# Kernel tuning notes

Hardware: AMD Instinct MI355X
Metric: run time of the kernel (lower is better)

## Reference

```python
import jax, jax.numpy as jnp
import numpy as np

N_NODES = 50000
N_EDGES = 800000
EMBED_ROWS = 100000
NUM_RELS = 16
NUM_BASES = 4
FEAT_DIM = 32
OUT_DIM = 32
ATTN_DIM = 32


def setup_inputs() -> dict:
    key = jax.random.key(0)
    ks = jax.random.split(key, 16)
    inp = {
        'feat': jax.random.normal(ks[0], (N_NODES, FEAT_DIM), jnp.float32),
        'embed_table': jax.random.normal(ks[1], (EMBED_ROWS, FEAT_DIM), jnp.float32),
        'transform': jax.random.normal(ks[2], (FEAT_DIM * 2, OUT_DIM), jnp.float32) * 0.1,
        'weight': jax.random.normal(ks[3], (NUM_BASES, OUT_DIM, OUT_DIM), jnp.float32) * 0.1,
        'w_comp': jax.random.normal(ks[4], (NUM_RELS, NUM_BASES), jnp.float32) * 0.5,
        'self_loop_weight': jax.random.normal(ks[5], (OUT_DIM, OUT_DIM), jnp.float32) * 0.1,
        'A_w': jax.random.normal(ks[6], (2 * OUT_DIM + ATTN_DIM, OUT_DIM), jnp.float32) * 0.1,
        'A_b': jax.random.normal(ks[7], (OUT_DIM,), jnp.float32) * 0.1,
        'B_w': jax.random.normal(ks[8], (OUT_DIM, 1), jnp.float32) * 0.1,
        'B_b': jax.random.normal(ks[9], (1,), jnp.float32) * 0.1,
        'attn_emb': jax.random.normal(ks[10], (NUM_RELS, ATTN_DIM), jnp.float32),
        'idx': jax.random.randint(ks[11], (N_NODES,), 0, EMBED_ROWS, jnp.int32),
        'edge_src': jax.random.randint(ks[12], (N_EDGES,), 0, N_NODES, jnp.int32),
        'edge_dst': jax.random.randint(ks[13], (N_EDGES,), 0, N_NODES, jnp.int32),
        'edge_type': jax.random.randint(ks[14], (N_EDGES,), 0, NUM_RELS, jnp.int32),
    }
    return inp


def reference(feat, embed_table, transform, weight, w_comp, self_loop_weight,
              A_w, A_b, B_w, B_b, attn_emb, idx, edge_src, edge_dst, edge_type):
    n = feat.shape[0]
    # input-layer features: concat(feat, embed[idx]) @ transform -> init_fea [N, D]
    init_fea = jnp.concatenate([feat, embed_table[idx]], axis=1) @ transform
    # basis decomposition: rel_w [R, D, D]
    rel_w = jnp.einsum('rb,bio->rio', w_comp, weight)
    # per-edge gather (is_input_layer & add_transe_emb -> x=src init_fea, y=dst init_fea)
    x = init_fea[edge_src]                      # [E, D]
    y = init_fea[edge_dst]                      # [E, D]
    w_e = rel_w[edge_type]                      # [E, D, D]
    msg = jnp.einsum('ed,edo->eo', x, w_e)      # per-edge bmm (edge weight w = 1)
    # attention MLP: a = sigmoid(B(relu(A([x, y, rel_emb]))))
    e = jnp.concatenate([x, y, attn_emb[edge_type]], axis=1)  # [E, 2D+A]
    a = jax.nn.sigmoid(jax.nn.relu(e @ A_w + A_b) @ B_w + B_b)  # [E, 1]
    # scatter-reduce: h_v = curr_emb_v + sum_{e: dst=v} a_e * msg_e
    agg = jax.ops.segment_sum(a * msg, edge_dst, num_segments=n)
    curr = init_fea @ self_loop_weight
    h = jax.nn.relu(curr + agg)  # activation=relu, bias=None, dropout=0
    # is_input_layer & add_transe_emb: repr = concat(init_fea, h) -> [N, 2, D]
    return jnp.stack([init_fea, h], axis=1)
```

## Files before the change

kernel.cpp:

```cpp
#include <hip/hip_runtime.h>
#include <math.h>

#define NN 50000
#define NE 800000
#define NR 16
#define BNODE 64
#define NBC 782
#define ABLK 256
#define CHUNK ((NE + ABLK - 1) / ABLK)
#define NTILE (NE / 16)

typedef __attribute__((ext_vector_type(8))) short short8;
typedef __attribute__((ext_vector_type(4))) float floatx4;

__device__ __forceinline__ unsigned short f2bf(float x) {
    unsigned int u = __float_as_uint(x);
    u += 0x7fffu + ((u >> 16) & 1u);
    return (unsigned short)(u >> 16);
}
__device__ __forceinline__ float bf2f(unsigned short s) {
    return __uint_as_float(((unsigned int)s) << 16);
}

__global__ void __launch_bounds__(256) k_pre(
    const float* __restrict__ feat, const float* __restrict__ emb,
    const float* __restrict__ T, const int* __restrict__ idx,
    const float* __restrict__ weight, const float* __restrict__ A_w,
    const float* __restrict__ A_b, const float* __restrict__ attn_emb,
    const int* __restrict__ ed,
    float* __restrict__ out, unsigned short* __restrict__ init_bf,
    unsigned short* __restrict__ bfrag, unsigned short* __restrict__ afrag,
    float* __restrict__ aproj, int* __restrict__ cpb) {
    if (blockIdx.x >= 260) {
        __shared__ int lc[NBC];
        const int cb = blockIdx.x - 260;
        for (int i = threadIdx.x; i < NBC; i += 256) lc[i] = 0;
        __syncthreads();
        const int start = cb * CHUNK, end = min(start + CHUNK, NE);
        for (int e = start + threadIdx.x; e < end; e += 256)
            atomicAdd(&lc[ed[e] >> 6], 1);
        __syncthreads();
        for (int i = threadIdx.x; i < NBC; i += 256) cpb[cb * NBC + i] = lc[i];
        return;
    }
    if (blockIdx.x < 64) {
        int g = blockIdx.x * 256 + threadIdx.x;
        if (g < 4 * 2 * 64 * 8) {
            int b2 = g >> 10, rest = g & 1023;
            int h = rest >> 9, l = (rest >> 3) & 63, j = rest & 7;
            int k = (l >> 4) * 8 + j, n = (l & 15) + 16 * h;
            bfrag[g] = f2bf(weight[b2 * 1024 + k * 32 + n]);
        }
        if (g < 2 * 2 * 64 * 8) {
            int ks = g >> 10, rest = g & 1023;
            int nt = rest >> 9, l = (rest >> 3) & 63, j = rest & 7;
            int k = ks * 32 + (l >> 4) * 8 + j, n = (l & 15) + 16 * nt;
            afrag[g] = f2bf(A_w[k * 32 + n]);
        }
        if (g < 16 * 32) {
            int t = g >> 5, j = g & 31;
            float acc = A_b[j];
#pragma unroll
            for (int k = 0; k < 32; k++) acc += attn_emb[t * 32 + k] * A_w[(64 + k) * 32 + j];
            aproj[g] = acc;
        }
        return;
    }
    int i = (blockIdx.x - 64) * 256 + threadIdx.x;
    if (i >= NN) return;
    float v[32], acc[32];
#pragma unroll
    for (int o = 0; o < 32; o++) acc[o] = 0.f;
    const float4* fp = (const float4*)(feat + (size_t)i * 32);
#pragma unroll
    for (int q = 0; q < 8; q++) {
        float4 f = fp[q];
        v[4 * q] = f.x; v[4 * q + 1] = f.y; v[4 * q + 2] = f.z; v[4 * q + 3] = f.w;
    }
#pragma unroll
    for (int d = 0; d < 32; d++) {
        float xd = v[d];
#pragma unroll
        for (int o = 0; o < 32; o++) acc[o] += xd * T[d * 32 + o];
    }
    int row = idx[i];
    const float4* ep = (const float4*)(emb + (size_t)row * 32);
#pragma unroll
    for (int q = 0; q < 8; q++) {
        float4 f = ep[q];
        v[4 * q] = f.x; v[4 * q + 1] = f.y; v[4 * q + 2] = f.z; v[4 * q + 3] = f.w;
    }
#pragma unroll
    for (int d = 0; d < 32; d++) {
        float xd = v[d];
#pragma unroll
        for (int o = 0; o < 32; o++) acc[o] += xd * T[(32 + d) * 32 + o];
    }
    float4* op = (float4*)(out + (size_t)i * 64);
#pragma unroll
    for (int q = 0; q < 8; q++) {
        float4 f;
        f.x = acc[4 * q]; f.y = acc[4 * q + 1]; f.z = acc[4 * q + 2]; f.w = acc[4 * q + 3];
        op[q] = f;
    }
    unsigned int w[16];
#pragma unroll
    for (int q = 0; q < 16; q++)
        w[q] = (unsigned int)f2bf(acc[2 * q]) | ((unsigned int)f2bf(acc[2 * q + 1]) << 16);
    uint4* bp = (uint4*)(init_bf + (size_t)i * 32);
#pragma unroll
    for (int q = 0; q < 4; q++) {
        uint4 u; u.x = w[4 * q]; u.y = w[4 * q + 1]; u.z = w[4 * q + 2]; u.w = w[4 * q + 3];
        bp[q] = u;
    }
}

__global__ void __launch_bounds__(256) k_scan1(const int* __restrict__ cpb,
                                               int* __restrict__ cpbx,
                                               int* __restrict__ tot) {
    int bin = blockIdx.x * 256 + threadIdx.x;
    if (bin >= NBC) return;
    int run = 0;
#pragma unroll 8
    for (int c = 0; c < ABLK; c++) {
        int v = cpb[c * NBC + bin];
        cpbx[c * NBC + bin] = run;
        run += v;
    }
    tot[bin] = run;
}

__global__ void __launch_bounds__(1024) k_scan2(const int* __restrict__ tot,
                                                int* __restrict__ boff) {
    __shared__ int ls[1024];
    int t = threadIdx.x;
    int v = (t < NBC) ? tot[t] : 0;
    ls[t] = v;
    __syncthreads();
    for (int off = 1; off < 1024; off <<= 1) {
        int u = (t >= off) ? ls[t - off] : 0;
        __syncthreads();
        ls[t] += u;
        __syncthreads();
    }
    if (t < NBC) boff[t] = ls[t] - v;
    if (t == NBC - 1) boff[NBC] = ls[t];
}

__global__ void __launch_bounds__(1024) k_scatA(const int* __restrict__ es,
                                                const int* __restrict__ ed,
                                                const int* __restrict__ et,
                                                const int* __restrict__ cpbx,
                                                const int* __restrict__ boff,
                                                int* __restrict__ bpack) {
    __shared__ int cur[NBC];
    const int start = blockIdx.x * CHUNK, end = min(start + CHUNK, NE);
    for (int i = threadIdx.x; i < NBC; i += 1024)
        cur[i] = boff[i] + cpbx[blockIdx.x * NBC + i];
    __syncthreads();
    for (int e = start + threadIdx.x; e < end; e += 1024) {
        int s = es[e], d = ed[e], t = et[e];
        int slot = atomicAdd(&cur[d >> 6], 1);
        bpack[slot] = s | ((d & 63) << 16) | (t << 22);
    }
}

__global__ void __launch_bounds__(256) k_fine(const int* __restrict__ boff,
                                              const int* __restrict__ bpack,
                                              int* __restrict__ row_off,
                                              int* __restrict__ e1,
                                              unsigned short* __restrict__ e2) {
    __shared__ int h[BNODE], ls[BNODE], cur[BNODE];
    const int b = blockIdx.x, tid = threadIdx.x;
    const int s0 = boff[b], s1 = boff[b + 1];
    if (tid < BNODE) h[tid] = 0;
    __syncthreads();
    for (int s = s0 + tid; s < s1; s += 256)
        atomicAdd(&h[(bpack[s] >> 16) & 63], 1);
    __syncthreads();
    if (tid < BNODE) ls[tid] = h[tid];
    __syncthreads();
    for (int off = 1; off < BNODE; off <<= 1) {
        int u = (tid < BNODE && tid >= off) ? ls[tid - off] : 0;
        __syncthreads();
        if (tid < BNODE) ls[tid] += u;
        __syncthreads();
    }
    if (tid < BNODE) {
        int excl = ls[tid] - h[tid];
        int node = b * BNODE + tid;
        if (node <= NN) row_off[node] = s0 + excl;
        cur[tid] = s0 + excl;
    }
    __syncthreads();
    for (int s = s0 + tid; s < s1; s += 256) {
        int pk = bpack[s];
        int f = (pk >> 16) & 63;
        int p = atomicAdd(&cur[f], 1);
        e1[p] = (pk & 0xffff) | (((pk >> 22) & 15) << 16);
        e2[p] = (unsigned short)(b * BNODE + f);
    }
}

__global__ void __launch_bounds__(256) k_msg(
    const unsigned short* __restrict__ bfrag, const unsigned short* __restrict__ afrag,
    const float* __restrict__ aproj, const float* __restrict__ w_comp,
    const float* __restrict__ B_w, const float* __restrict__ B_b,
    const int* __restrict__ e1, const unsigned short* __restrict__ e2,
    const unsigned short* __restrict__ init_bf, unsigned short* __restrict__ amsg) {
    const int wave = threadIdx.x >> 6;
    const int lane = threadIdx.x & 63;
    const int ti = blockIdx.x * 4 + wave;
    const int m = lane & 15, quad = lane >> 4;
    const int e = ti * 16 + m;
    const int ev = e1[e];
    const int src = ev & 0xffff;
    const int dst = e2[e];
    short8 xa = *(const short8*)(init_bf + (size_t)src * 32 + quad * 8);
    short8 ya = *(const short8*)(init_bf + (size_t)dst * 32 + quad * 8);
    const short8* bfp = (const short8*)bfrag;
    const short8* afp = (const short8*)afrag;
    floatx4 z4 = {0.f, 0.f, 0.f, 0.f};
    floatx4 hc0 = __builtin_amdgcn_mfma_f32_16x16x32_bf16(xa, afp[0 * 64 + lane], z4, 0, 0, 0);
    hc0 = __builtin_amdgcn_mfma_f32_16x16x32_bf16(ya, afp[2 * 64 + lane], hc0, 0, 0, 0);
    floatx4 hc1 = __builtin_amdgcn_mfma_f32_16x16x32_bf16(xa, afp[1 * 64 + lane], z4, 0, 0, 0);
    hc1 = __builtin_amdgcn_mfma_f32_16x16x32_bf16(ya, afp[3 * 64 + lane], hc1, 0, 0, 0);
    int tr[4];
    float4 wcr[4];
#pragma unroll
    for (int r = 0; r < 4; r++) {
        int evr = __shfl(ev, quad * 20 + r, 64);
        tr[r] = (evr >> 16) & 15;
        wcr[r] = ((const float4*)w_comp)[tr[r]];
    }
    floatx4 m0 = z4, m1 = z4;
#pragma unroll
    for (int bs = 0; bs < 4; bs++) {
        floatx4 zb0 = __builtin_amdgcn_mfma_f32_16x16x32_bf16(xa, bfp[(2 * bs) * 64 + lane], z4, 0, 0, 0);
        floatx4 zb1 = __builtin_amdgcn_mfma_f32_16x16x32_bf16(xa, bfp[(2 * bs + 1) * 64 + lane], z4, 0, 0, 0);
#pragma unroll
        for (int r = 0; r < 4; r++) {
            float w = (bs == 0) ? wcr[r].x : (bs == 1) ? wcr[r].y : (bs == 2) ? wcr[r].z : wcr[r].w;
            m0[r] += w * zb0[r];
            m1[r] += w * zb1[r];
        }
    }
    const float bw0 = B_w[m], bw1 = B_w[m + 16], bb = B_b[0];
    float part[4];
#pragma unroll
    for (int r = 0; r < 4; r++)
        part[r] = fmaxf(hc0[r] + aproj[tr[r] * 32 + m], 0.f) * bw0
                + fmaxf(hc1[r] + aproj[tr[r] * 32 + 16 + m], 0.f) * bw1;
#pragma unroll
    for (int s = 1; s < 16; s <<= 1) {
#pragma unroll
        for (int r = 0; r < 4; r++) part[r] += __shfl_xor(part[r], s, 64);
    }
#pragma unroll
    for (int r = 0; r < 4; r++) {
        const int p = ti * 16 + quad * 4 + r;
        float a = 1.f / (1.f + __expf(-(part[r] + bb)));
        amsg[(size_t)p * 32 + m] = f2bf(a * m0[r]);
        amsg[(size_t)p * 32 + m + 16] = f2bf(a * m1[r]);
    }
}

__global__ void __launch_bounds__(256) k_agg(
    const int* __restrict__ row_off, const unsigned short* __restrict__ amsg,
    const float* __restrict__ S, float* __restrict__ out) {
    int tid = threadIdx.x;
    int v = blockIdx.x * 64 + (tid >> 2);
    if (v >= NN) return;
    int c0 = (tid & 3) * 8;
    float acc[8];
#pragma unroll
    for (int j = 0; j < 8; j++) acc[j] = 0.f;
    int p0 = row_off[v], p1 = row_off[v + 1];
    for (int p = p0; p < p1; p++) {
        short8 mv = *(const short8*)(amsg + (size_t)p * 32 + c0);
#pragma unroll
        for (int j = 0; j < 8; j++) acc[j] += bf2f((unsigned short)mv[j]);
    }
    float x[32];
    const float4* xp = (const float4*)(out + (size_t)v * 64);
#pragma unroll
    for (int q = 0; q < 8; q++) {
        float4 f = xp[q];
        x[4 * q] = f.x; x[4 * q + 1] = f.y; x[4 * q + 2] = f.z; x[4 * q + 3] = f.w;
    }
#pragma unroll
    for (int d = 0; d < 32; d++) {
        float xd = x[d];
#pragma unroll
        for (int j = 0; j < 8; j++) acc[j] += xd * S[d * 32 + c0 + j];
    }
    float4* op = (float4*)(out + (size_t)v * 64 + 32 + c0);
#pragma unroll
    for (int q = 0; q < 2; q++) {
        float4 f;
        f.x = fmaxf(acc[4 * q], 0.f);
        f.y = fmaxf(acc[4 * q + 1], 0.f);
        f.z = fmaxf(acc[4 * q + 2], 0.f);
        f.w = fmaxf(acc[4 * q + 3], 0.f);
        op[q] = f;
    }
}

extern "C" void kernel_launch(void* const* d_in, const int* in_sizes, int n_in,
                              void* d_out, int out_size, void* d_ws, size_t ws_size,
                              hipStream_t stream) {
    const float* feat      = (const float*)d_in[0];
    const float* embed     = (const float*)d_in[1];
    const float* transform = (const float*)d_in[2];
    const float* weight    = (const float*)d_in[3];
    const float* w_comp    = (const float*)d_in[4];
    const float* self_w    = (const float*)d_in[5];
    const float* A_w       = (const float*)d_in[6];
    const float* A_b       = (const float*)d_in[7];
    const float* B_w       = (const float*)d_in[8];
    const float* B_b       = (const float*)d_in[9];
    const float* attn_emb  = (const float*)d_in[10];
    const int*   idx       = (const int*)d_in[11];
    const int*   edge_src  = (const int*)d_in[12];
    const int*   edge_dst  = (const int*)d_in[13];
    const int*   edge_type = (const int*)d_in[14];
    float* out = (float*)d_out;

    char* ws = (char*)d_ws;
    unsigned short* amsg    = (unsigned short*)ws;
    int*            bpack   = (int*)ws;
    unsigned short* init_bf = (unsigned short*)(ws + (size_t)NE * 64);
    unsigned short* bfrag   = (unsigned short*)((char*)init_bf + 3200000);
    unsigned short* afrag   = (unsigned short*)((char*)bfrag + 8192);
    float*          aproj   = (float*)((char*)afrag + 4096);
    int* ip      = (int*)((char*)aproj + 2048);
    int* boff    = ip;            ip += NBC + 2;
    int* tot     = ip;            ip += 1024;
    int* cpb     = ip;            ip += ABLK * NBC;
    int* cpbx    = ip;            ip += ABLK * NBC;
    int* row_off = ip;            ip += NN + 1;
    int* e1      = ip;            ip += NE;
    unsigned short* e2 = (unsigned short*)ip;

    k_pre<<<516, 256, 0, stream>>>(feat, embed, transform, idx, weight,
                                   A_w, A_b, attn_emb, edge_dst,
                                   out, init_bf, bfrag, afrag, aproj, cpb);
    k_scan1<<<4, 256, 0, stream>>>(cpb, cpbx, tot);
    k_scan2<<<1, 1024, 0, stream>>>(tot, boff);
    k_scatA<<<ABLK, 1024, 0, stream>>>(edge_src, edge_dst, edge_type, cpbx, boff, bpack);
    k_fine<<<NBC, 256, 0, stream>>>(boff, bpack, row_off, e1, e2);
    k_msg<<<NTILE / 4, 256, 0, stream>>>(bfrag, afrag, aproj, w_comp, B_w, B_b,
                                         e1, e2, init_bf, amsg);
    k_agg<<<(NN + 63) / 64, 256, 0, stream>>>(row_off, amsg, self_w, out);
}
```

Baseline: 214.2 us.

## Process multiple edge tiles per wave with prefetch and packed message stores

```diff
diff --git a/kernel.cpp b/kernel.cpp
--- a/kernel.cpp
+++ b/kernel.cpp
@@ -9,6 +9,7 @@
 #define ABLK 256
 #define CHUNK ((NE + ABLK - 1) / ABLK)
 #define NTILE (NE / 16)
+#define TPW 4
 
 typedef __attribute__((ext_vector_type(8))) short short8;
 typedef __attribute__((ext_vector_type(4))) float floatx4;
@@ -207,79 +208,120 @@
     const float* __restrict__ aproj, const float* __restrict__ w_comp,
     const float* __restrict__ B_w, const float* __restrict__ B_b,
     const int* __restrict__ e1, const unsigned short* __restrict__ e2,
-    const unsigned short* __restrict__ init_bf, unsigned short* __restrict__ amsg) {
+    const unsigned short* __restrict__ init_bf, unsigned int* __restrict__ amsg32) {
     const int wave = threadIdx.x >> 6;
     const int lane = threadIdx.x & 63;
-    const int ti = blockIdx.x * 4 + wave;
     const int m = lane & 15, quad = lane >> 4;
-    const int e = ti * 16 + m;
-    const int ev = e1[e];
-    const int src = ev & 0xffff;
-    const int dst = e2[e];
-    short8 xa = *(const short8*)(init_bf + (size_t)src * 32 + quad * 8);
-    short8 ya = *(const short8*)(init_bf + (size_t)dst * 32 + quad * 8);
+    const int t0 = (blockIdx.x * 4 + wave) * TPW;
     const short8* bfp = (const short8*)bfrag;
     const short8* afp = (const short8*)afrag;
-    floatx4 z4 = {0.f, 0.f, 0.f, 0.f};
-    floatx4 hc0 = __builtin_amdgcn_mfma_f32_16x16x32_bf16(xa, afp[0 * 64 + lane], z4, 0, 0, 0);
-    hc0 = __builtin_amdgcn_mfma_f32_16x16x32_bf16(ya, afp[2 * 64 + lane], hc0, 0, 0, 0);
-    floatx4 hc1 = __builtin_amdgcn_mfma_f32_16x16x32_bf16(xa, afp[1 * 64 + lane], z4, 0, 0, 0);
-    hc1 = __builtin_amdgcn_mfma_f32_16x16x32_bf16(ya, afp[3 * 64 + lane], hc1, 0, 0, 0);
-    int tr[4];
-    float4 wcr[4];
-#pragma unroll
-    for (int r = 0; r < 4; r++) {
-        int evr = __shfl(ev, quad * 20 + r, 64);
-        tr[r] = (evr >> 16) & 15;
-        wcr[r] = ((const float4*)w_comp)[tr[r]];
-    }
-    floatx4 m0 = z4, m1 = z4;
-#pragma unroll
-    for (int bs = 0; bs < 4; bs++) {
-        floatx4 zb0 = __builtin_amdgcn_mfma_f32_16x16x32_bf16(xa, bfp[(2 * bs) * 64 + lane], z4, 0, 0, 0);
-        floatx4 zb1 = __builtin_amdgcn_mfma_f32_16x16x32_bf16(xa, bfp[(2 * bs + 1) * 64 + lane], z4, 0, 0, 0);
+    short8 af0 = afp[0 * 64 + lane], af1 = afp[1 * 64 + lane];
+    short8 af2 = afp[2 * 64 + lane], af3 = afp[3 * 64 + lane];
+    short8 bf0 = bfp[0 * 64 + lane], bf1 = bfp[1 * 64 + lane];
+    short8 bf2 = bfp[2 * 64 + lane], bf3 = bfp[3 * 64 + lane];
+    short8 bf4 = bfp[4 * 64 + lane], bf5 = bfp[5 * 64 + lane];
+    short8 bf6 = bfp[6 * 64 + lane], bf7 = bfp[7 * 64 + lane];
+    const float bw0 = B_w[m], bw1 = B_w[m + 16], bb = B_b[0];
+    const unsigned short* ibq = init_bf + quad * 8;
+    int ev[TPW]; int dv[TPW];
+#pragma unroll
+    for (int t = 0; t < TPW; t++) {
+        ev[t] = e1[(t0 + t) * 16 + m];
+        dv[t] = e2[(t0 + t) * 16 + m];
+    }
+    short8 xa = *(const short8*)(ibq + (size_t)(ev[0] & 0xffff) * 32);
+    short8 ya = *(const short8*)(ibq + (size_t)dv[0] * 32);
+    const short8 z8 = {0, 0, 0, 0, 0, 0, 0, 0};
+#pragma unroll
+    for (int t = 0; t < TPW; t++) {
+        short8 xan = z8, yan = z8;
+        if (t + 1 < TPW) {
+            xan = *(const short8*)(ibq + (size_t)(ev[t + 1] & 0xffff) * 32);
+            yan = *(const short8*)(ibq + (size_t)dv[t + 1] * 32);
+        }
+        int tr[4];
+        float4 wcr[4];
 #pragma unroll
         for (int r = 0; r < 4; r++) {
-            float w = (bs == 0) ? wcr[r].x : (bs == 1) ? wcr[r].y : (bs == 2) ? wcr[r].z : wcr[r].w;
-            m0[r] += w * zb0[r];
-            m1[r] += w * zb1[r];
-        }
-    }
-    const float bw0 = B_w[m], bw1 = B_w[m + 16], bb = B_b[0];
-    float part[4];
-#pragma unroll
-    for (int r = 0; r < 4; r++)
-        part[r] = fmaxf(hc0[r] + aproj[tr[r] * 32 + m], 0.f) * bw0
-                + fmaxf(hc1[r] + aproj[tr[r] * 32 + 16 + m], 0.f) * bw1;
-#pragma unroll
-    for (int s = 1; s < 16; s <<= 1) {
-#pragma unroll
-        for (int r = 0; r < 4; r++) part[r] += __shfl_xor(part[r], s, 64);
-    }
-#pragma unroll
-    for (int r = 0; r < 4; r++) {
-        const int p = ti * 16 + quad * 4 + r;
-        float a = 1.f / (1.f + __expf(-(part[r] + bb)));
-        amsg[(size_t)p * 32 + m] = f2bf(a * m0[r]);
-        amsg[(size_t)p * 32 + m + 16] = f2bf(a * m1[r]);
+            int evr = __shfl(ev[t], quad * 20 + r, 64);
+            tr[r] = (evr >> 16) & 15;
+            wcr[r] = ((const float4*)w_comp)[tr[r]];
+        }
+        floatx4 z4 = {0.f, 0.f, 0.f, 0.f};
+        floatx4 hc0 = __builtin_amdgcn_mfma_f32_16x16x32_bf16(xa, af0, z4, 0, 0, 0);
+        hc0 = __builtin_amdgcn_mfma_f32_16x16x32_bf16(ya, af2, hc0, 0, 0, 0);
+        floatx4 hc1 = __builtin_amdgcn_mfma_f32_16x16x32_bf16(xa, af1, z4, 0, 0, 0);
+        hc1 = __builtin_amdgcn_mfma_f32_16x16x32_bf16(ya, af3, hc1, 0, 0, 0);
+        floatx4 m0 = z4, m1 = z4;
+        {
+            floatx4 zb0 = __builtin_amdgcn_mfma_f32_16x16x32_bf16(xa, bf0, z4, 0, 0, 0);
+            floatx4 zb1 = __builtin_amdgcn_mfma_f32_16x16x32_bf16(xa, bf1, z4, 0, 0, 0);
+#pragma unroll
+            for (int r = 0; r < 4; r++) { m0[r] += wcr[r].x * zb0[r]; m1[r] += wcr[r].x * zb1[r]; }
+        }
+        {
+            floatx4 zb0 = __builtin_amdgcn_mfma_f32_16x16x32_bf16(xa, bf2, z4, 0, 0, 0);
+            floatx4 zb1 = __builtin_amdgcn_mfma_f32_16x16x32_bf16(xa, bf3, z4, 0, 0, 0);
+#pragma unroll
+            for (int r = 0; r < 4; r++) { m0[r] += wcr[r].y * zb0[r]; m1[r] += wcr[r].y * zb1[r]; }
+        }
+        {
+            floatx4 zb0 = __builtin_amdgcn_mfma_f32_16x16x32_bf16(xa, bf4, z4, 0, 0, 0);
+            floatx4 zb1 = __builtin_amdgcn_mfma_f32_16x16x32_bf16(xa, bf5, z4, 0, 0, 0);
+#pragma unroll
+            for (int r = 0; r < 4; r++) { m0[r] += wcr[r].z * zb0[r]; m1[r] += wcr[r].z * zb1[r]; }
+        }
+        {
+            floatx4 zb0 = __builtin_amdgcn_mfma_f32_16x16x32_bf16(xa, bf6, z4, 0, 0, 0);
+            floatx4 zb1 = __builtin_amdgcn_mfma_f32_16x16x32_bf16(xa, bf7, z4, 0, 0, 0);
+#pragma unroll
+            for (int r = 0; r < 4; r++) { m0[r] += wcr[r].w * zb0[r]; m1[r] += wcr[r].w * zb1[r]; }
+        }
+        float part[4];
+#pragma unroll
+        for (int r = 0; r < 4; r++)
+            part[r] = fmaxf(hc0[r] + aproj[tr[r] * 32 + m], 0.f) * bw0
+                    + fmaxf(hc1[r] + aproj[tr[r] * 32 + 16 + m], 0.f) * bw1;
+#pragma unroll
+        for (int s = 1; s < 16; s <<= 1) {
+#pragma unroll
+            for (int r = 0; r < 4; r++) part[r] += __shfl_xor(part[r], s, 64);
+        }
+        const int ti = t0 + t;
+#pragma unroll
+        for (int r = 0; r < 4; r++) {
+            const int p = ti * 16 + quad * 4 + r;
+            float a = 1.f / (1.f + __expf(-(part[r] + bb)));
+            unsigned int pk = (unsigned int)f2bf(a * m0[r])
+                            | ((unsigned int)f2bf(a * m1[r]) << 16);
+            amsg32[(size_t)p * 16 + m] = pk;
+        }
+        xa = xan; ya = yan;
     }
 }
 
 __global__ void __launch_bounds__(256) k_agg(
-    const int* __restrict__ row_off, const unsigned short* __restrict__ amsg,
+    const int* __restrict__ row_off, const unsigned int* __restrict__ amsg32,
     const float* __restrict__ S, float* __restrict__ out) {
     int tid = threadIdx.x;
     int v = blockIdx.x * 64 + (tid >> 2);
     if (v >= NN) return;
     int c0 = (tid & 3) * 8;
+    const int base = c0 & 8;
+    const bool hi = c0 >= 16;
     float acc[8];
 #pragma unroll
     for (int j = 0; j < 8; j++) acc[j] = 0.f;
     int p0 = row_off[v], p1 = row_off[v + 1];
     for (int p = p0; p < p1; p++) {
-        short8 mv = *(const short8*)(amsg + (size_t)p * 32 + c0);
-#pragma unroll
-        for (int j = 0; j < 8; j++) acc[j] += bf2f((unsigned short)mv[j]);
+        const uint4* rp = (const uint4*)(amsg32 + (size_t)p * 16 + base);
+        uint4 u0 = rp[0], u1 = rp[1];
+        unsigned int uu[8] = {u0.x, u0.y, u0.z, u0.w, u1.x, u1.y, u1.z, u1.w};
+#pragma unroll
+        for (int j = 0; j < 8; j++) {
+            unsigned int raw = hi ? (uu[j] & 0xffff0000u) : (uu[j] << 16);
+            acc[j] += __uint_as_float(raw);
+        }
     }
     float x[32];
     const float4* xp = (const float4*)(out + (size_t)v * 64);
@@ -327,7 +369,7 @@
     float* out = (float*)d_out;
 
     char* ws = (char*)d_ws;
-    unsigned short* amsg    = (unsigned short*)ws;
+    unsigned int*   amsg32  = (unsigned int*)ws;
     int*            bpack   = (int*)ws;
     unsigned short* init_bf = (unsigned short*)(ws + (size_t)NE * 64);
     unsigned short* bfrag   = (unsigned short*)((char*)init_bf + 3200000);
@@ -349,7 +391,7 @@
     k_scan2<<<1, 1024, 0, stream>>>(tot, boff);
     k_scatA<<<ABLK, 1024, 0, stream>>>(edge_src, edge_dst, edge_type, cpbx, boff, bpack);
     k_fine<<<NBC, 256, 0, stream>>>(boff, bpack, row_off, e1, e2);
-    k_msg<<<NTILE / 4, 256, 0, stream>>>(bfrag, afrag, aproj, w_comp, B_w, B_b,
-                                         e1, e2, init_bf, amsg);
-    k_agg<<<(NN + 63) / 64, 256, 0, stream>>>(row_off, amsg, self_w, out);
-}
+    k_msg<<<NTILE / (4 * TPW), 256, 0, stream>>>(bfrag, afrag, aproj, w_comp, B_w, B_b,
+                                                 e1, e2, init_bf, amsg32);
+    k_agg<<<(NN + 63) / 64, 256, 0, stream>>>(row_off, amsg32, self_w, out);
+}
```

Measured after the change: 209.3 us. -2.3%, faster.
